# Optimization experiments

Measured on AMD Instinct MI355X. Metric: run time of the kernel, lower is better.

The kernel has to match this reference:

```python
import jax, jax.numpy as jnp
import numpy as np
from jax import lax

S = 2048      # seq_len
E = 512       # loc_emb_size
H = 512       # hidden_size
V = 50000     # loc_size
WIN = 11      # window: j in [i-10, i]
LAMBDA_T = 0.1
LAMBDA_S = 50.0
DAY = 86400.0


def setup_inputs() -> dict:
    key = jax.random.key(0)
    ks = jax.random.split(key, 10)
    loc = jax.random.randint(ks[0], (S, 1), 0, V)
    # monotonically increasing timestamps spanning ~1 week
    tim = jnp.sort(jax.random.uniform(ks[1], (S,), dtype=jnp.float32) * (7.0 * DAY))
    coord = jax.random.uniform(ks[2], (S, 2), dtype=jnp.float32)
    emb = jax.random.normal(ks[3], (V, E), dtype=jnp.float32) * 0.02
    s_e = 1.0 / np.sqrt(E)
    s_h = 1.0 / np.sqrt(H)
    W_ih = jax.random.normal(ks[4], (3 * H, E), dtype=jnp.float32) * s_e
    W_hh = jax.random.normal(ks[5], (3 * H, H), dtype=jnp.float32) * s_h
    b_ih = jnp.zeros((3 * H,), dtype=jnp.float32)
    b_hh = jnp.zeros((3 * H,), dtype=jnp.float32)
    fc_w = jax.random.normal(ks[6], (V, H), dtype=jnp.float32) * s_h
    fc_b = jnp.zeros((V,), dtype=jnp.float32)
    return {"loc": loc, "tim": tim, "coord": coord, "emb": emb,
            "W_ih": W_ih, "W_hh": W_hh, "b_ih": b_ih, "b_hh": b_hh,
            "fc_w": fc_w, "fc_b": fc_b}


def _gru(x, W_ih, W_hh, b_ih, b_hh):
    # x: [S, E] -> out: [S, H]; PyTorch GRU equations (batch=1, 1 layer)
    xg = x @ W_ih.T + b_ih  # [S, 3H] precomputed input gates
    h0 = jnp.zeros((H,), dtype=x.dtype)

    def step(h, xg_t):
        hg = h @ W_hh.T + b_hh
        xr, xz, xn = jnp.split(xg_t, 3)
        hr, hz, hn = jnp.split(hg, 3)
        r = jax.nn.sigmoid(xr + hr)
        z = jax.nn.sigmoid(xz + hz)
        n = jnp.tanh(xn + r * hn)
        h_new = (1.0 - z) * n + z * h
        return h_new, h_new

    _, out = lax.scan(step, h0, xg)
    return out


def _flashback_core(out, tim, coord):
    # windowed spatiotemporal-decay weighted aggregation, fully vectorized
    i = jnp.arange(S)
    d = jnp.arange(WIN)                      # offsets 0..10
    j = i[:, None] - d[None, :]
    valid = j >= 0
    jc = jnp.maximum(j, 0)
    dt = tim[:, None] - tim[jc]
    diff = coord[:, None, :] - coord[jc]
    sq = jnp.sum(diff * diff, axis=-1)
    ds = jnp.sqrt(jnp.where(sq > 0, sq, 1.0)) * (sq > 0)  # safe norm (grad 0 at 0)
    f_t = (jnp.cos(dt * (2.0 * np.pi / DAY)) + 1.0) * 0.5 * jnp.exp(-(dt / DAY) * LAMBDA_T)
    f_s = jnp.exp(-ds * LAMBDA_S)
    w = jnp.where(valid, f_t * f_s + 1e-10, 0.0)
    out_w = jnp.einsum('sw,swh->sh', w, out[jc]) / jnp.sum(w, axis=1, keepdims=True)
    return out_w


def reference(loc, tim, coord, emb, W_ih, W_hh, b_ih, b_hh, fc_w, fc_b):
    x = emb[loc[:, 0]]                       # [S, E] (dropout is identity in eval)
    out = _gru(x, W_ih, W_hh, b_ih, b_hh)    # [S, H]
    out_w = _flashback_core(out, tim, coord) # [S, H]
    h = jax.nn.selu(out_w)
    y = h @ fc_w.T + fc_b                    # [S, V]
    return jax.nn.log_softmax(y, axis=-1)
```

## Files before the change

### kernel.cpp

```cpp
#include <hip/hip_runtime.h>
#include <math.h>

#define S_DIM 2048
#define H_DIM 512
#define V_DIM 50000
#define K_DIM 512
#define WINN 11
#define GRU_G 32

typedef __attribute__((ext_vector_type(4))) float f32x4;
typedef __attribute__((ext_vector_type(8))) __bf16 bf16x8;
typedef __attribute__((ext_vector_type(4))) unsigned int u32x4;

__device__ __forceinline__ unsigned int f2bf(float f) {
  union { float f; unsigned int u; } v; v.f = f;
  return (v.u + 0x7fffu + ((v.u >> 16) & 1u)) >> 16;
}
__device__ __forceinline__ unsigned int pack2(float a, float b) {
  return f2bf(a) | (f2bf(b) << 16);
}

__global__ void k_zero(int* p, int n) {
  int i = blockIdx.x * 256 + threadIdx.x;
  if (i < n) p[i] = 0;
}

__global__ void k_swizzle(const float* __restrict__ src, unsigned short* __restrict__ dst,
                          int rows_valid, int nchunks) {
  int c = blockIdx.x * 256 + threadIdx.x;
  if (c >= nchunks) return;
  int vt  = c >> 13;
  int m   = (c >> 6) & 127;
  int ktq = c & 63;
  int v = vt * 128 + m;
  f32x4 a = {0, 0, 0, 0}, b = {0, 0, 0, 0};
  if (v < rows_valid) {
    const float* s = src + (size_t)v * K_DIM + ktq * 8;
    a = *(const f32x4*)s;
    b = *(const f32x4*)(s + 4);
  }
  u32x4 pk;
  pk.x = pack2(a.x, a.y); pk.y = pack2(a.z, a.w);
  pk.z = pack2(b.x, b.y); pk.w = pack2(b.z, b.w);
  int kt = ktq >> 2, q = ktq & 3;
  int cd = vt * 8192 + kt * 512 + q * 128 + m;
  *(u32x4*)(dst + (size_t)cd * 8) = pk;
}

__global__ void k_gather(const float* __restrict__ emb, const int* __restrict__ loc,
                         unsigned short* __restrict__ dst) {
  int c = blockIdx.x * 256 + threadIdx.x;
  int st  = c >> 13;
  int m   = (c >> 6) & 127;
  int ktq = c & 63;
  int s = st * 128 + m;
  int l = loc[s];
  const float* sp = emb + (size_t)l * K_DIM + ktq * 8;
  f32x4 a = *(const f32x4*)sp;
  f32x4 b = *(const f32x4*)(sp + 4);
  u32x4 pk;
  pk.x = pack2(a.x, a.y); pk.y = pack2(a.z, a.w);
  pk.z = pack2(b.x, b.y); pk.w = pack2(b.z, b.w);
  int kt = ktq >> 2, q = ktq & 3;
  int cd = st * 8192 + kt * 512 + q * 128 + m;
  *(u32x4*)(dst + (size_t)cd * 8) = pk;
}

__global__ __launch_bounds__(256) void k_gemm(const unsigned short* __restrict__ A,
                                              const unsigned short* __restrict__ B,
                                              const float* __restrict__ bias,
                                              float* __restrict__ C, int ldc, int nvalid) {
  __shared__ __align__(16) unsigned short Als[4096];
  __shared__ __align__(16) unsigned short Bls[4096];
  int t = threadIdx.x;
  int ntile = blockIdx.x, mtile = blockIdx.y;
  const unsigned short* Ab = A + (size_t)mtile * 65536;
  const unsigned short* Bb = B + (size_t)ntile * 65536;
  int wid = t >> 6, lane = t & 63;
  int qm = wid >> 1, qn = wid & 1;
  int l15 = lane & 15, q4 = lane >> 4;
  f32x4 acc[4][4];
#pragma unroll
  for (int i = 0; i < 4; i++)
#pragma unroll
    for (int j = 0; j < 4; j++) acc[i][j] = (f32x4){0, 0, 0, 0};

  for (int kt = 0; kt < 16; ++kt) {
    __syncthreads();
    ((u32x4*)Als)[t]       = ((const u32x4*)(Ab + kt * 4096))[t];
    ((u32x4*)Als)[t + 256] = ((const u32x4*)(Ab + kt * 4096))[t + 256];
    ((u32x4*)Bls)[t]       = ((const u32x4*)(Bb + kt * 4096))[t];
    ((u32x4*)Bls)[t + 256] = ((const u32x4*)(Bb + kt * 4096))[t + 256];
    __syncthreads();
    bf16x8 af[4], bfr[4];
#pragma unroll
    for (int i = 0; i < 4; i++)
      af[i] = *(const bf16x8*)(&Als[(q4 * 128 + qm * 64 + i * 16 + l15) * 8]);
#pragma unroll
    for (int j = 0; j < 4; j++)
      bfr[j] = *(const bf16x8*)(&Bls[(q4 * 128 + qn * 64 + j * 16 + l15) * 8]);
#pragma unroll
    for (int i = 0; i < 4; i++)
#pragma unroll
      for (int j = 0; j < 4; j++)
        acc[i][j] = __builtin_amdgcn_mfma_f32_16x16x32_bf16(af[i], bfr[j], acc[i][j], 0, 0, 0);
  }

  int m0 = mtile * 128 + qm * 64;
  int n0 = ntile * 128 + qn * 64;
#pragma unroll
  for (int j = 0; j < 4; j++) {
    int n = n0 + j * 16 + l15;
    if (n < nvalid) {
      float bv = bias[n];
#pragma unroll
      for (int i = 0; i < 4; i++) {
        int r = m0 + i * 16 + q4 * 4;
#pragma unroll
        for (int e = 0; e < 4; e++)
          C[(size_t)(r + e) * ldc + n] = acc[i][j][e] + bv;
      }
    }
  }
}

__global__ __launch_bounds__(256, 1) void k_gru(const float* __restrict__ W_hh,
                                                const float* __restrict__ b_hh,
                                                const float* __restrict__ xg,
                                                unsigned long long* h_pairs,
                                                float* __restrict__ out_gru) {
  __shared__ __align__(16) float h_lds[512];
  __shared__ float hg_l[48];
  int g = blockIdx.x;
  int t = threadIdx.x;
  int r = t >> 2, kq = t & 3;
  bool act = (t < 192);
  f32x4 wr[32];
  float bhh = 0.f;
  if (act) {
    int grow = (r >> 4) * 512 + g * 16 + (r & 15);
    const float* wsrc = W_hh + (size_t)grow * K_DIM + kq * 128;
#pragma unroll
    for (int c = 0; c < 32; c++) wr[c] = *(const f32x4*)(wsrc + c * 4);
    bhh = b_hh[grow];
  }
  int mycol = g * 16 + t;
  float ho = 0.f;

  for (int s = 0; s < S_DIM; ++s) {
    float xr = 0.f, xz = 0.f, xn = 0.f;
    if (t < 16) {
      const float* xrow = xg + (size_t)s * 1536;
      xr = xrow[mycol];
      xz = xrow[512 + mycol];
      xn = xrow[1024 + mycol];
    }

    unsigned long long* slot = h_pairs + (size_t)(s & 1) * 512;
    unsigned long long u0 = __hip_atomic_load(slot + t,       __ATOMIC_RELAXED, __HIP_MEMORY_SCOPE_AGENT);
    unsigned long long u1 = __hip_atomic_load(slot + t + 256, __ATOMIC_RELAXED, __HIP_MEMORY_SCOPE_AGENT);
    while ((unsigned)(u0 >> 32) != (unsigned)s)
      u0 = __hip_atomic_load(slot + t,       __ATOMIC_RELAXED, __HIP_MEMORY_SCOPE_AGENT);
    while ((unsigned)(u1 >> 32) != (unsigned)s)
      u1 = __hip_atomic_load(slot + t + 256, __ATOMIC_RELAXED, __HIP_MEMORY_SCOPE_AGENT);
    union { unsigned uu; float ff; } c0, c1;
    c0.uu = (unsigned)u0; c1.uu = (unsigned)u1;
    h_lds[t]       = c0.ff;
    h_lds[t + 256] = c1.ff;
    __syncthreads();

    if (act) {
      const f32x4* h4 = ((const f32x4*)h_lds) + kq * 32;
      float p0 = 0.f, p1 = 0.f, p2 = 0.f, p3 = 0.f;
#pragma unroll
      for (int c = 0; c < 32; c += 4) {
        f32x4 h0 = h4[c], h1 = h4[c + 1], h2 = h4[c + 2], h3 = h4[c + 3];
        p0 += wr[c].x * h0.x + wr[c].y * h0.y + wr[c].z * h0.z + wr[c].w * h0.w;
        p1 += wr[c + 1].x * h1.x + wr[c + 1].y * h1.y + wr[c + 1].z * h1.z + wr[c + 1].w * h1.w;
        p2 += wr[c + 2].x * h2.x + wr[c + 2].y * h2.y + wr[c + 2].z * h2.z + wr[c + 2].w * h2.w;
        p3 += wr[c + 3].x * h3.x + wr[c + 3].y * h3.y + wr[c + 3].z * h3.z + wr[c + 3].w * h3.w;
      }
      float a0 = (p0 + p1) + (p2 + p3);
      a0 += __shfl_xor(a0, 1, 64);
      a0 += __shfl_xor(a0, 2, 64);
      if (kq == 0) hg_l[r] = a0 + bhh;
    }
    __syncthreads();

    if (t < 16) {
      int i = t;
      float hr = hg_l[i], hz = hg_l[16 + i], hn = hg_l[32 + i];
      float rg = 1.f / (1.f + expf(-(xr + hr)));
      float zg = 1.f / (1.f + expf(-(xz + hz)));
      float nn = tanhf(xn + rg * hn);
      float hnew = (1.f - zg) * nn + zg * ho;
      out_gru[(size_t)s * H_DIM + mycol] = hnew;
      union { float ff; unsigned uu; } pv; pv.ff = hnew;
      unsigned long long up = ((unsigned long long)(unsigned)(s + 1) << 32) | (unsigned long long)pv.uu;
      __hip_atomic_store(h_pairs + (size_t)((s + 1) & 1) * 512 + mycol, up,
                         __ATOMIC_RELAXED, __HIP_MEMORY_SCOPE_AGENT);
      ho = hnew;
    }
  }
}

__global__ __launch_bounds__(256) void k_flash(const float* __restrict__ out_gru,
                                               const float* __restrict__ tim,
                                               const float* __restrict__ coord,
                                               unsigned short* __restrict__ hs_sw) {
  __shared__ float hsl[512];
  int s = blockIdx.x;
  int t = threadIdx.x;
  float w[WINN];
  float ts = tim[s];
  float cx = coord[s * 2], cy = coord[s * 2 + 1];
  float wsum = 0.f;
#pragma unroll
  for (int d = 0; d < WINN; ++d) {
    int j = s - d;
    float wd = 0.f;
    if (j >= 0) {
      float dt = ts - tim[j];
      float dx = cx - coord[j * 2], dy = cy - coord[j * 2 + 1];
      float sq = dx * dx + dy * dy;
      float ds = sq > 0.f ? sqrtf(sq) : 0.f;
      float ft = (cosf(dt * 7.2722052166430395e-05f) + 1.f) * 0.5f *
                 expf(dt * -1.1574074074074074e-06f);
      float fs = expf(-50.f * ds);
      wd = ft * fs + 1e-10f;
    }
    w[d] = wd;
    wsum += wd;
  }
  float inv = 1.f / wsum;
  for (int h = t; h < H_DIM; h += 256) {
    float a = 0.f;
#pragma unroll
    for (int d = 0; d < WINN; ++d) {
      int j = s - d;
      if (j >= 0) a += w[d] * out_gru[(size_t)j * H_DIM + h];
    }
    a *= inv;
    float o = a > 0.f ? 1.0507009873554805f * a
                      : 1.7580993408473766f * expm1f(a);
    hsl[h] = o;
  }
  __syncthreads();
  if (t < 64) {
    int kt = t >> 2, q = t & 3;
    const float* p = &hsl[t * 8];
    u32x4 pk;
    pk.x = pack2(p[0], p[1]); pk.y = pack2(p[2], p[3]);
    pk.z = pack2(p[4], p[5]); pk.w = pack2(p[6], p[7]);
    int st = s >> 7, m = s & 127;
    int cd = st * 8192 + kt * 512 + q * 128 + m;
    *(u32x4*)(hs_sw + (size_t)cd * 8) = pk;
  }
}

__global__ __launch_bounds__(256) void k_rowsum(const float* __restrict__ Y,
                                                float* __restrict__ lse) {
  __shared__ float red[256];
  int s = blockIdx.x, t = threadIdx.x;
  const float* row = Y + (size_t)s * V_DIM;
  float acc = 0.f;
  for (int v = t; v < V_DIM; v += 256) acc += expf(row[v]);
  red[t] = acc;
  __syncthreads();
  for (int o = 128; o > 0; o >>= 1) {
    if (t < o) red[t] += red[t + o];
    __syncthreads();
  }
  if (t == 0) lse[s] = logf(red[0]);
}

__global__ __launch_bounds__(256) void k_sub(float* __restrict__ Y,
                                             const float* __restrict__ lse) {
  int i = blockIdx.x * 256 + threadIdx.x;
  const int n4 = S_DIM * (V_DIM / 4);
  if (i >= n4) return;
  int row = (i * 4) / V_DIM;
  f32x4* Y4 = (f32x4*)Y;
  f32x4 v = Y4[i];
  float l = lse[row];
  v.x -= l; v.y -= l; v.z -= l; v.w -= l;
  Y4[i] = v;
}

extern "C" void kernel_launch(void* const* d_in, const int* in_sizes, int n_in,
                              void* d_out, int out_size, void* d_ws, size_t ws_size,
                              hipStream_t stream) {
  const int*   loc   = (const int*)d_in[0];
  const float* tim   = (const float*)d_in[1];
  const float* coord = (const float*)d_in[2];
  const float* emb   = (const float*)d_in[3];
  const float* W_ih  = (const float*)d_in[4];
  const float* W_hh  = (const float*)d_in[5];
  const float* b_ih  = (const float*)d_in[6];
  const float* b_hh  = (const float*)d_in[7];
  const float* fc_w  = (const float*)d_in[8];
  const float* fc_b  = (const float*)d_in[9];
  float* Y = (float*)d_out;

  char* w = (char*)d_ws;
  unsigned long long* h_pairs = (unsigned long long*)(w);
  float* lse     = (float*)(w + 8192);
  float* xg      = (float*)(w + 16384);
  float* out_gru = (float*)(w + 12599296);
  unsigned short* x_sw   = (unsigned short*)(w + 16793600);
  unsigned short* wih_sw = (unsigned short*)(w + 18890752);
  unsigned short* hs_sw  = (unsigned short*)(w + 20463616);
  unsigned short* fcw_sw = (unsigned short*)(w + 22560768);

  k_zero<<<8, 256, 0, stream>>>((int*)w, 2048);
  k_swizzle<<<12512, 256, 0, stream>>>(fc_w, fcw_sw, 50000, 391 * 8192);
  k_swizzle<<<384, 256, 0, stream>>>(W_ih, wih_sw, 1536, 12 * 8192);
  k_gather<<<512, 256, 0, stream>>>(emb, loc, x_sw);
  dim3 gx(12, 16);
  k_gemm<<<gx, 256, 0, stream>>>(x_sw, wih_sw, b_ih, xg, 1536, 1536);
  k_gru<<<GRU_G, 256, 0, stream>>>(W_hh, b_hh, xg, h_pairs, out_gru);
  k_flash<<<2048, 256, 0, stream>>>(out_gru, tim, coord, hs_sw);
  dim3 gy(391, 16);
  k_gemm<<<gy, 256, 0, stream>>>(hs_sw, fcw_sw, fc_b, Y, 50000, 50000);
  k_rowsum<<<2048, 256, 0, stream>>>(Y, lse);
  k_sub<<<100000, 256, 0, stream>>>(Y, lse);
}
```

Before: 5.370 ms.

## Restructure GRU step to 512 threads with wave-local gate reduction

The recurrent GRU kernel now uses 512 threads per block. Each wave computes the three gates for two hidden columns and reduces them with shuffles, so the second block barrier and the shared-memory gate staging are gone. The hidden state is double-buffered in LDS with an XOR swizzle to avoid bank conflicts. The spin-wait now keeps several atomic loads in flight at once. This shortens the serial per-timestep critical path, at the cost of more redundant polling loads and an idle fourth gate slot per wave.

```diff
diff --git a/kernel.cpp b/kernel.cpp
--- a/kernel.cpp
+++ b/kernel.cpp
@@ -18,6 +18,9 @@
 }
 __device__ __forceinline__ unsigned int pack2(float a, float b) {
   return f2bf(a) | (f2bf(b) << 16);
+}
+__device__ __forceinline__ unsigned long long ld_pair(const unsigned long long* p) {
+  return __hip_atomic_load(p, __ATOMIC_RELAXED, __HIP_MEMORY_SCOPE_AGENT);
 }
 
 __global__ void k_zero(int* p, int n) {
@@ -124,81 +127,89 @@
   }
 }
 
-__global__ __launch_bounds__(256, 1) void k_gru(const float* __restrict__ W_hh,
+__global__ __launch_bounds__(512, 1) void k_gru(const float* __restrict__ W_hh,
                                                 const float* __restrict__ b_hh,
                                                 const float* __restrict__ xg,
                                                 unsigned long long* h_pairs,
                                                 float* __restrict__ out_gru) {
-  __shared__ __align__(16) float h_lds[512];
-  __shared__ float hg_l[48];
+  __shared__ __align__(16) float h_lds[2][512];
   int g = blockIdx.x;
   int t = threadIdx.x;
-  int r = t >> 2, kq = t & 3;
-  bool act = (t < 192);
-  f32x4 wr[32];
+  int wv = t >> 6;
+  int lane = t & 63;
+  int cl = lane >> 5;
+  int rem = lane & 31;
+  int gate = rem >> 3;
+  int kq = rem & 7;
+  bool act = (gate < 3);
+  int col = g * 16 + wv * 2 + cl;
+  f32x4 wr[16];
   float bhh = 0.f;
   if (act) {
-    int grow = (r >> 4) * 512 + g * 16 + (r & 15);
-    const float* wsrc = W_hh + (size_t)grow * K_DIM + kq * 128;
-#pragma unroll
-    for (int c = 0; c < 32; c++) wr[c] = *(const f32x4*)(wsrc + c * 4);
+    int grow = gate * 512 + col;
+    const float* wsrc = W_hh + (size_t)grow * K_DIM + kq * 64;
+#pragma unroll
+    for (int c = 0; c < 16; c++) wr[c] = *(const f32x4*)(wsrc + c * 4);
     bhh = b_hh[grow];
   }
-  int mycol = g * 16 + t;
+  bool pub = (rem == 0);
   float ho = 0.f;
+  int wj = t >> 2;
+  int wp = ((wj ^ ((wj >> 4) & 7)) << 2) | (t & 3);
 
   for (int s = 0; s < S_DIM; ++s) {
     float xr = 0.f, xz = 0.f, xn = 0.f;
-    if (t < 16) {
+    if (pub) {
       const float* xrow = xg + (size_t)s * 1536;
-      xr = xrow[mycol];
-      xz = xrow[512 + mycol];
-      xn = xrow[1024 + mycol];
-    }
-
-    unsigned long long* slot = h_pairs + (size_t)(s & 1) * 512;
-    unsigned long long u0 = __hip_atomic_load(slot + t,       __ATOMIC_RELAXED, __HIP_MEMORY_SCOPE_AGENT);
-    unsigned long long u1 = __hip_atomic_load(slot + t + 256, __ATOMIC_RELAXED, __HIP_MEMORY_SCOPE_AGENT);
-    while ((unsigned)(u0 >> 32) != (unsigned)s)
-      u0 = __hip_atomic_load(slot + t,       __ATOMIC_RELAXED, __HIP_MEMORY_SCOPE_AGENT);
-    while ((unsigned)(u1 >> 32) != (unsigned)s)
-      u1 = __hip_atomic_load(slot + t + 256, __ATOMIC_RELAXED, __HIP_MEMORY_SCOPE_AGENT);
-    union { unsigned uu; float ff; } c0, c1;
-    c0.uu = (unsigned)u0; c1.uu = (unsigned)u1;
-    h_lds[t]       = c0.ff;
-    h_lds[t + 256] = c1.ff;
+      xr = xrow[col]; xz = xrow[512 + col]; xn = xrow[1024 + col];
+    }
+
+    unsigned long long* p = h_pairs + (size_t)(s & 1) * 512 + t;
+    unsigned long long b0 = ld_pair(p), b1 = ld_pair(p), b2 = ld_pair(p), b3 = ld_pair(p);
+    while ((unsigned)(b0 >> 32) != (unsigned)s) {
+      b0 = b1; b1 = b2; b2 = b3; b3 = ld_pair(p);
+    }
+    union { unsigned u; float f; } cv; cv.u = (unsigned)b0;
+    float* hb = h_lds[s & 1];
+    hb[wp] = cv.f;
     __syncthreads();
 
+    float a = 0.f;
     if (act) {
-      const f32x4* h4 = ((const f32x4*)h_lds) + kq * 32;
+      const f32x4* h4 = (const f32x4*)hb;
       float p0 = 0.f, p1 = 0.f, p2 = 0.f, p3 = 0.f;
 #pragma unroll
-      for (int c = 0; c < 32; c += 4) {
-        f32x4 h0 = h4[c], h1 = h4[c + 1], h2 = h4[c + 2], h3 = h4[c + 3];
+      for (int c = 0; c < 16; c += 4) {
+        f32x4 h0 = h4[(kq * 16 + c)     ^ kq];
+        f32x4 h1 = h4[(kq * 16 + c + 1) ^ kq];
+        f32x4 h2 = h4[(kq * 16 + c + 2) ^ kq];
+        f32x4 h3 = h4[(kq * 16 + c + 3) ^ kq];
         p0 += wr[c].x * h0.x + wr[c].y * h0.y + wr[c].z * h0.z + wr[c].w * h0.w;
         p1 += wr[c + 1].x * h1.x + wr[c + 1].y * h1.y + wr[c + 1].z * h1.z + wr[c + 1].w * h1.w;
         p2 += wr[c + 2].x * h2.x + wr[c + 2].y * h2.y + wr[c + 2].z * h2.z + wr[c + 2].w * h2.w;
         p3 += wr[c + 3].x * h3.x + wr[c + 3].y * h3.y + wr[c + 3].z * h3.z + wr[c + 3].w * h3.w;
       }
-      float a0 = (p0 + p1) + (p2 + p3);
-      a0 += __shfl_xor(a0, 1, 64);
-      a0 += __shfl_xor(a0, 2, 64);
-      if (kq == 0) hg_l[r] = a0 + bhh;
-    }
-    __syncthreads();
-
-    if (t < 16) {
-      int i = t;
-      float hr = hg_l[i], hz = hg_l[16 + i], hn = hg_l[32 + i];
+      a = (p0 + p1) + (p2 + p3);
+    }
+    a += __shfl_xor(a, 1, 64);
+    a += __shfl_xor(a, 2, 64);
+    a += __shfl_xor(a, 4, 64);
+    a += bhh;
+    int base = cl << 5;
+    float hr = __shfl(a, base,      64);
+    float hz = __shfl(a, base + 8,  64);
+    float hn = __shfl(a, base + 16, 64);
+    if (pub) {
       float rg = 1.f / (1.f + expf(-(xr + hr)));
       float zg = 1.f / (1.f + expf(-(xz + hz)));
       float nn = tanhf(xn + rg * hn);
       float hnew = (1.f - zg) * nn + zg * ho;
-      out_gru[(size_t)s * H_DIM + mycol] = hnew;
-      union { float ff; unsigned uu; } pv; pv.ff = hnew;
-      unsigned long long up = ((unsigned long long)(unsigned)(s + 1) << 32) | (unsigned long long)pv.uu;
-      __hip_atomic_store(h_pairs + (size_t)((s + 1) & 1) * 512 + mycol, up,
+      union { float f; unsigned u; } pv; pv.f = hnew;
+      unsigned long long up = ((unsigned long long)(unsigned)(s + 1) << 32) |
+                              (unsigned long long)pv.u;
+      __hip_atomic_store(h_pairs + (size_t)((s + 1) & 1) * 512 + col, up,
                          __ATOMIC_RELAXED, __HIP_MEMORY_SCOPE_AGENT);
+      out_gru[(size_t)s * H_DIM + col] = hnew;
       ho = hnew;
     }
   }
@@ -318,7 +329,7 @@
   k_gather<<<512, 256, 0, stream>>>(emb, loc, x_sw);
   dim3 gx(12, 16);
   k_gemm<<<gx, 256, 0, stream>>>(x_sw, wih_sw, b_ih, xg, 1536, 1536);
-  k_gru<<<GRU_G, 256, 0, stream>>>(W_hh, b_hh, xg, h_pairs, out_gru);
+  k_gru<<<GRU_G, 512, 0, stream>>>(W_hh, b_hh, xg, h_pairs, out_gru);
   k_flash<<<2048, 256, 0, stream>>>(out_gru, tim, coord, hs_sw);
   dim3 gy(391, 16);
   k_gemm<<<gy, 256, 0, stream>>>(hs_sw, fcw_sw, fc_b, Y, 50000, 50000);
```

New measurement: 7.040 ms. +31.1%, slower.
